# Performance work log

Hardware: AMD Instinct MI355X
Metric: run time of the kernel (lower is better)

The kernel has to match this reference:

```python
import jax, jax.numpy as jnp
import numpy as np

MARGIN = 1.0
EPS = 1e-12


def setup_inputs() -> dict:
    key = jax.random.key(0)
    k1, k2, k3 = jax.random.split(key, 3)
    inputs = jax.random.normal(k1, (8192, 128), dtype=jnp.float32)
    targets = jax.random.randint(k2, (8192,), 0, 64, dtype=jnp.int64)
    center = jax.random.normal(k3, (16, 128), dtype=jnp.float32)
    return {"inputs": inputs, "targets": targets, "center": center}


def reference(inputs, targets, center):
    n = inputs.shape[0]
    # pairwise Euclidean distances via ||a||^2 + ||b||^2 - 2 a.b  (matches addmm_ trick)
    sq = jnp.sum(inputs * inputs, axis=1)                      # [n]
    dist2 = sq[:, None] + sq[None, :] - 2.0 * (inputs @ inputs.T)
    dist = jnp.sqrt(jnp.clip(dist2, EPS))                      # [n, n]

    mask = targets[:, None] == targets[None, :]                # same-class mask [n, n]

    # batch-hard mining, fully vectorized (replaces per-row python loops)
    dist_ap = jnp.max(jnp.where(mask, dist, -jnp.inf), axis=1)  # hardest positive
    neg_min = jnp.min(jnp.where(mask, jnp.inf, dist), axis=1)   # hardest negative
    has_neg = jnp.any(~mask, axis=1)
    dist_an = jnp.where(has_neg, neg_min, dist_ap + MARGIN)

    # center augmentation: min over distances to L2-normalized prototypes
    cn = center / jnp.linalg.norm(center, axis=1, keepdims=True)       # [P, d]
    dc = jnp.sqrt(jnp.sum((inputs[:, None, :] - cn[None, :, :]) ** 2, axis=-1))  # [n, P]
    dc = jnp.clip(dc, EPS)
    dist_an = jnp.minimum(dist_an, jnp.min(dc, axis=1))

    # MarginRankingLoss with y=1: mean(relu(dist_ap - dist_an + margin))
    loss = jnp.mean(jnp.maximum(dist_ap - dist_an + MARGIN, 0.0))
    return loss
```

## Files before the change

### kernel.cpp

```cpp
#include <hip/hip_runtime.h>
#include <hip/hip_bf16.h>


#define N_ROWS 8192
#define DIM 128
#define NPROTO 16
#define MARGIN_F 1.0f
#define EPS_F 1e-12f

typedef __attribute__((ext_vector_type(8))) short short8;
typedef __attribute__((ext_vector_type(4))) float float4v;

static __device__ __forceinline__ unsigned f2bf(float f) {
  unsigned u = __float_as_uint(f);
  u += 0x7fffu + ((u >> 16) & 1u);
  return u >> 16;
}

__global__ void prep_centers_kernel(const float* __restrict__ center,
                                    float* __restrict__ cn,
                                    float* __restrict__ out0) {
  int tid = threadIdx.x;
  if (tid == 0) out0[0] = 0.0f;
  int row = tid >> 4;
  int l = tid & 15;
  float v[8];
  float ss = 0.f;
#pragma unroll
  for (int j = 0; j < 8; ++j) {
    v[j] = center[row * DIM + l * 8 + j];
    ss += v[j] * v[j];
  }
#pragma unroll
  for (int m = 1; m < 16; m <<= 1) ss += __shfl_xor(ss, m, 64);
  float inv = 1.0f / sqrtf(ss);
#pragma unroll
  for (int j = 0; j < 8; ++j) cn[row * DIM + l * 8 + j] = v[j] * inv;
}

__global__ void prep_rows_kernel(const float* __restrict__ x,
                                 const float* __restrict__ cn,
                                 uint4* __restrict__ xbf4,
                                 float* __restrict__ sq,
                                 float* __restrict__ mindc) {
  __shared__ float scn[NPROTO * DIM];
  int tid = threadIdx.x;
#pragma unroll
  for (int j = 0; j < 8; ++j) scn[j * 256 + tid] = cn[j * 256 + tid];
  __syncthreads();
  int rloc = tid >> 4, l = tid & 15;
  int row = blockIdx.x * 16 + rloc;
  float4 v0 = ((const float4*)x)[row * 32 + l * 2];
  float4 v1 = ((const float4*)x)[row * 32 + l * 2 + 1];
  float ss = v0.x * v0.x + v0.y * v0.y + v0.z * v0.z + v0.w * v0.w +
             v1.x * v1.x + v1.y * v1.y + v1.z * v1.z + v1.w * v1.w;
  float dots[NPROTO];
#pragma unroll
  for (int p = 0; p < NPROTO; ++p) {
    const float* c = &scn[p * DIM + l * 8];
    dots[p] = v0.x * c[0] + v0.y * c[1] + v0.z * c[2] + v0.w * c[3] +
              v1.x * c[4] + v1.y * c[5] + v1.z * c[6] + v1.w * c[7];
  }
#pragma unroll
  for (int m = 1; m < 16; m <<= 1) {
    ss += __shfl_xor(ss, m, 64);
#pragma unroll
    for (int p = 0; p < NPROTO; ++p) dots[p] += __shfl_xor(dots[p], m, 64);
  }
  uint4 pk;
  pk.x = f2bf(v0.x) | (f2bf(v0.y) << 16);
  pk.y = f2bf(v0.z) | (f2bf(v0.w) << 16);
  pk.z = f2bf(v1.x) | (f2bf(v1.y) << 16);
  pk.w = f2bf(v1.z) | (f2bf(v1.w) << 16);
  xbf4[row * 16 + l] = pk;
  if (l == 0) {
    float mind2 = INFINITY;
#pragma unroll
    for (int p = 0; p < NPROTO; ++p)
      mind2 = fminf(mind2, ss + 1.0f - 2.0f * dots[p]);
    sq[row] = ss;
    mindc[row] = fmaxf(sqrtf(fmaxf(mind2, 0.0f)), EPS_F);
  }
}

__global__ __launch_bounds__(256, 2) void
pairdist_kernel(const char* __restrict__ xbf, const float* __restrict__ sq,
                const int* __restrict__ tgt, float* __restrict__ pmax,
                float* __restrict__ pmin) {
  __shared__ float smax[4][64];
  __shared__ float smin[4][64];
  int bid = blockIdx.x;
  int rg = bid >> 3;
  int strip = bid & 7;
  int wave = threadIdx.x >> 6, lane = threadIdx.x & 63;
  int rowbase = rg * 64;
  int q = lane >> 4, l16 = lane & 15;
  int colbase = strip * 1024 + wave * 256;

  short8 a[4][4];
#pragma unroll
  for (int rt = 0; rt < 4; ++rt) {
    const char* ar = xbf + (size_t)(rowbase + rt * 16 + l16) * 256 + q * 16;
#pragma unroll
    for (int kc = 0; kc < 4; ++kc) a[rt][kc] = *(const short8*)(ar + kc * 64);
  }
  int4 trow[4];
#pragma unroll
  for (int rt = 0; rt < 4; ++rt)
    trow[rt] = ((const int4*)tgt)[(rowbase >> 2) + rt * 4 + q];

  float maxp[16], minn[16];
#pragma unroll
  for (int i = 0; i < 16; ++i) { maxp[i] = -INFINITY; minn[i] = INFINITY; }

  short8 bn[4];
  float sqn;
  int tcn;
  {
    const char* br = xbf + (size_t)(colbase + l16) * 256 + q * 16;
#pragma unroll
    for (int kc = 0; kc < 4; ++kc) bn[kc] = *(const short8*)(br + kc * 64);
    sqn = sq[colbase + l16];
    tcn = tgt[colbase + l16];
  }

#pragma unroll
  for (int t = 0; t < 16; ++t) {
    short8 bc[4];
#pragma unroll
    for (int kc = 0; kc < 4; ++kc) bc[kc] = bn[kc];
    float sqc = sqn;
    int tc = tcn;
    int cnext = colbase + ((t + 1) & 15) * 16;
    const char* br = xbf + (size_t)(cnext + l16) * 256 + q * 16;
#pragma unroll
    for (int kc = 0; kc < 4; ++kc) bn[kc] = *(const short8*)(br + kc * 64);
    sqn = sq[cnext + l16];
    tcn = tgt[cnext + l16];

    float4v acc[4];
#pragma unroll
    for (int rt = 0; rt < 4; ++rt) acc[rt] = (float4v){0.f, 0.f, 0.f, 0.f};
#pragma unroll
    for (int kc = 0; kc < 4; ++kc)
#pragma unroll
      for (int rt = 0; rt < 4; ++rt)
        acc[rt] = __builtin_amdgcn_mfma_f32_16x16x32_bf16(a[rt][kc], bc[kc],
                                                          acc[rt], 0, 0, 0);
#pragma unroll
    for (int rt = 0; rt < 4; ++rt) {
      int tr[4] = {trow[rt].x, trow[rt].y, trow[rt].z, trow[rt].w};
#pragma unroll
      for (int r = 0; r < 4; ++r) {
        float v = fmaf(-2.0f, acc[rt][r], sqc);
        bool s = (tc == tr[r]);
        int idx = rt * 4 + r;
        maxp[idx] = s ? fmaxf(maxp[idx], v) : maxp[idx];
        minn[idx] = s ? minn[idx] : fminf(minn[idx], v);
      }
    }
  }

#pragma unroll
  for (int m = 1; m < 16; m <<= 1) {
#pragma unroll
    for (int i = 0; i < 16; ++i) {
      maxp[i] = fmaxf(maxp[i], __shfl_xor(maxp[i], m, 64));
      minn[i] = fminf(minn[i], __shfl_xor(minn[i], m, 64));
    }
  }
  if (l16 == 0) {
#pragma unroll
    for (int rt = 0; rt < 4; ++rt)
#pragma unroll
      for (int r = 0; r < 4; ++r) {
        smax[wave][rt * 16 + q * 4 + r] = maxp[rt * 4 + r];
        smin[wave][rt * 16 + q * 4 + r] = minn[rt * 4 + r];
      }
  }
  __syncthreads();
  if (threadIdx.x < 64) {
    float M = fmaxf(fmaxf(smax[0][threadIdx.x], smax[1][threadIdx.x]),
                    fmaxf(smax[2][threadIdx.x], smax[3][threadIdx.x]));
    float m = fminf(fminf(smin[0][threadIdx.x], smin[1][threadIdx.x]),
                    fminf(smin[2][threadIdx.x], smin[3][threadIdx.x]));
    pmax[strip * N_ROWS + rowbase + threadIdx.x] = M;
    pmin[strip * N_ROWS + rowbase + threadIdx.x] = m;
  }
}

__global__ void finalize_kernel(const float* __restrict__ pmax,
                                const float* __restrict__ pmin,
                                const float* __restrict__ sq,
                                const float* __restrict__ mindc,
                                float* __restrict__ out) {
  __shared__ float wsum[4];
  int i = blockIdx.x * 256 + threadIdx.x;
  float maxv = -INFINITY, minv = INFINITY;
#pragma unroll
  for (int s = 0; s < 8; ++s) {
    maxv = fmaxf(maxv, pmax[s * N_ROWS + i]);
    minv = fminf(minv, pmin[s * N_ROWS + i]);
  }
  float si = sq[i];
  float dap = sqrtf(fmaxf(si + maxv, EPS_F));
  float dan = (minv > 1e37f) ? (dap + MARGIN_F) : sqrtf(fmaxf(si + minv, EPS_F));
  dan = fminf(dan, mindc[i]);
  float c = fmaxf(dap - dan + MARGIN_F, 0.0f) * (1.0f / (float)N_ROWS);
#pragma unroll
  for (int m = 1; m < 64; m <<= 1) c += __shfl_xor(c, m, 64);
  int lane = threadIdx.x & 63, wave = threadIdx.x >> 6;
  if (lane == 0) wsum[wave] = c;
  __syncthreads();
  if (threadIdx.x == 0) atomicAdd(out, wsum[0] + wsum[1] + wsum[2] + wsum[3]);
}

extern "C" void kernel_launch(void* const* d_in, const int* in_sizes, int n_in,
                              void* d_out, int out_size, void* d_ws, size_t ws_size,
                              hipStream_t stream) {
  const float* inputs = (const float*)d_in[0];
  const int* targets = (const int*)d_in[1];
  const float* center = (const float*)d_in[2];
  char* ws = (char*)d_ws;
  uint4* xbf4     = (uint4*)(ws + 0);
  float* sq       = (float*)(ws + 2097152);
  float* mindc    = (float*)(ws + 2129920);
  float* cn       = (float*)(ws + 2162688);
  float* pmax     = (float*)(ws + 2170880);
  float* pmin     = (float*)(ws + 2433024);
  float* out      = (float*)d_out;

  prep_centers_kernel<<<1, 256, 0, stream>>>(center, cn, out);
  prep_rows_kernel<<<512, 256, 0, stream>>>(inputs, cn, xbf4, sq, mindc);
  pairdist_kernel<<<1024, 256, 0, stream>>>((const char*)xbf4, sq, targets, pmax, pmin);
  finalize_kernel<<<32, 256, 0, stream>>>(pmax, pmin, sq, mindc, out);
}
```

Baseline: 111.4 us.

## Encode class mask into extra GEMM K-dims, stage column tiles via LDS

Each row gets 64 extra bf16 K-columns holding a one-hot class code scaled so that same-class pairs pick up a large bias in the dot product. A plain max and min over the biased distances then separates positives from negatives without per-element target compares, and finalize removes the bias. Column tiles are now loaded into swizzled, double-buffered LDS with global_load_lds and shared by four waves. The center prep kernel is merged into the row prep kernel. The cost is a K dimension of 192 instead of 128 (50% more MFMA work), per-tile block barriers, and a bias of 32768 that coarsens fp32 precision of the positive distances.

```diff
diff --git a/kernel.cpp b/kernel.cpp
--- a/kernel.cpp
+++ b/kernel.cpp
@@ -1,15 +1,18 @@
 #include <hip/hip_runtime.h>
-#include <hip/hip_bf16.h>
 
 
 #define N_ROWS 8192
 #define DIM 128
+#define KDIM 192
+#define ROWB 384
 #define NPROTO 16
 #define MARGIN_F 1.0f
 #define EPS_F 1e-12f
+#define BIAS_F 32768.0f
 
 typedef __attribute__((ext_vector_type(8))) short short8;
 typedef __attribute__((ext_vector_type(4))) float float4v;
+typedef __attribute__((ext_vector_type(4))) unsigned uint4v;
 
 static __device__ __forceinline__ unsigned f2bf(float f) {
   unsigned u = __float_as_uint(f);
@@ -17,38 +20,39 @@
   return u >> 16;
 }
 
-__global__ void prep_centers_kernel(const float* __restrict__ center,
-                                    float* __restrict__ cn,
-                                    float* __restrict__ out0) {
-  int tid = threadIdx.x;
-  if (tid == 0) out0[0] = 0.0f;
-  int row = tid >> 4;
-  int l = tid & 15;
-  float v[8];
-  float ss = 0.f;
-#pragma unroll
-  for (int j = 0; j < 8; ++j) {
-    v[j] = center[row * DIM + l * 8 + j];
-    ss += v[j] * v[j];
-  }
-#pragma unroll
-  for (int m = 1; m < 16; m <<= 1) ss += __shfl_xor(ss, m, 64);
-  float inv = 1.0f / sqrtf(ss);
-#pragma unroll
-  for (int j = 0; j < 8; ++j) cn[row * DIM + l * 8 + j] = v[j] * inv;
-}
-
-__global__ void prep_rows_kernel(const float* __restrict__ x,
-                                 const float* __restrict__ cn,
-                                 uint4* __restrict__ xbf4,
-                                 float* __restrict__ sq,
-                                 float* __restrict__ mindc) {
+static __device__ __forceinline__ void gload_lds16(const void* g, void* l) {
+  __builtin_amdgcn_global_load_lds(
+      (const __attribute__((address_space(1))) unsigned*)g,
+      (__attribute__((address_space(3))) unsigned*)l, 16, 0, 0);
+}
+
+__global__ void prep_kernel(const float* __restrict__ x,
+                            const float* __restrict__ center,
+                            const int* __restrict__ tgt,
+                            char* __restrict__ xbf,
+                            float* __restrict__ sq,
+                            float* __restrict__ mindc,
+                            float* __restrict__ out) {
   __shared__ float scn[NPROTO * DIM];
   int tid = threadIdx.x;
-#pragma unroll
-  for (int j = 0; j < 8; ++j) scn[j * 256 + tid] = cn[j * 256 + tid];
+  if (blockIdx.x == 0 && tid == 0) out[0] = 0.0f;
+  int rloc = tid >> 4, l = tid & 15;
+  {
+    float v[8];
+    float ss = 0.f;
+#pragma unroll
+    for (int j = 0; j < 8; ++j) {
+      v[j] = center[rloc * DIM + l * 8 + j];
+      ss += v[j] * v[j];
+    }
+#pragma unroll
+    for (int m = 1; m < 16; m <<= 1) ss += __shfl_xor(ss, m, 64);
+    float inv = 1.0f / sqrtf(ss);
+#pragma unroll
+    for (int j = 0; j < 8; ++j) scn[rloc * DIM + l * 8 + j] = v[j] * inv;
+  }
   __syncthreads();
-  int rloc = tid >> 4, l = tid & 15;
+
   int row = blockIdx.x * 16 + rloc;
   float4 v0 = ((const float4*)x)[row * 32 + l * 2];
   float4 v1 = ((const float4*)x)[row * 32 + l * 2 + 1];
@@ -72,7 +76,17 @@
   pk.y = f2bf(v0.z) | (f2bf(v0.w) << 16);
   pk.z = f2bf(v1.x) | (f2bf(v1.y) << 16);
   pk.w = f2bf(v1.z) | (f2bf(v1.w) << 16);
-  xbf4[row * 16 + l] = pk;
+  *(uint4*)(xbf + (size_t)row * ROWB + l * 16) = pk;
+  int cls = tgt[row];
+  if (l < 8) {
+    unsigned wv = (cls & 1) ? 0xC3000000u : 0x0000C300u;
+    uint4 oh;
+    oh.x = ((cls >> 1) == (l * 4 + 0)) ? wv : 0u;
+    oh.y = ((cls >> 1) == (l * 4 + 1)) ? wv : 0u;
+    oh.z = ((cls >> 1) == (l * 4 + 2)) ? wv : 0u;
+    oh.w = ((cls >> 1) == (l * 4 + 3)) ? wv : 0u;
+    *(uint4*)(xbf + (size_t)row * ROWB + 256 + l * 16) = oh;
+  }
   if (l == 0) {
     float mind2 = INFINITY;
 #pragma unroll
@@ -85,107 +99,109 @@
 
 __global__ __launch_bounds__(256, 2) void
 pairdist_kernel(const char* __restrict__ xbf, const float* __restrict__ sq,
-                const int* __restrict__ tgt, float* __restrict__ pmax,
-                float* __restrict__ pmin) {
-  __shared__ float smax[4][64];
-  __shared__ float smin[4][64];
-  int bid = blockIdx.x;
-  int rg = bid >> 3;
-  int strip = bid & 7;
-  int wave = threadIdx.x >> 6, lane = threadIdx.x & 63;
-  int rowbase = rg * 64;
-  int q = lane >> 4, l16 = lane & 15;
-  int colbase = strip * 1024 + wave * 256;
-
-  short8 a[4][4];
+                float* __restrict__ pmax, float* __restrict__ pmin) {
+  __shared__ __align__(16) char bl[2][6144];
+  const int bid = blockIdx.x;
+  const int rg = bid >> 4;
+  const int strip = bid & 15;
+  const int wave = threadIdx.x >> 6, lane = threadIdx.x & 63;
+  const int q = lane >> 4, l16 = lane & 15;
+  const int rowbase = rg * 256 + wave * 64;
+  const int stripbase = strip * 512;
+
+  const int slot = wave * 64 + lane;
+  const char* const srcstrip = xbf + (size_t)stripbase * ROWB;
+  int op0 = slot * 16;
+  int c0 = op0 / ROWB;
+  const int soff0 = c0 * ROWB + ((op0 - c0 * ROWB) ^ ((c0 & 7) << 4));
+  int op1 = 4096 + slot * 16;
+  int c1 = op1 / ROWB;
+  const int soff1 = c1 * ROWB + ((op1 - c1 * ROWB) ^ ((c1 & 7) << 4));
+
+  auto stage = [&](int t, char* buf) {
+    const char* s = srcstrip + (size_t)t * 6144;
+    gload_lds16(s + soff0, buf + wave * 1024);
+    if (wave < 2) gload_lds16(s + soff1, buf + 4096 + wave * 1024);
+  };
+
+  stage(0, bl[0]);
+
+  short8 a[4][6];
 #pragma unroll
   for (int rt = 0; rt < 4; ++rt) {
-    const char* ar = xbf + (size_t)(rowbase + rt * 16 + l16) * 256 + q * 16;
-#pragma unroll
-    for (int kc = 0; kc < 4; ++kc) a[rt][kc] = *(const short8*)(ar + kc * 64);
-  }
-  int4 trow[4];
-#pragma unroll
-  for (int rt = 0; rt < 4; ++rt)
-    trow[rt] = ((const int4*)tgt)[(rowbase >> 2) + rt * 4 + q];
+    const char* ar = xbf + (size_t)(rowbase + rt * 16 + l16) * ROWB + q * 16;
+#pragma unroll
+    for (int kc = 0; kc < 6; ++kc) a[rt][kc] = *(const short8*)(ar + kc * 64);
+#pragma unroll
+    for (int kc = 4; kc < 6; ++kc) {
+      uint4v u = __builtin_bit_cast(uint4v, a[rt][kc]);
+      u ^= 0x80008000u;
+      a[rt][kc] = __builtin_bit_cast(short8, u);
+    }
+  }
+
+  int roff[6];
+#pragma unroll
+  for (int kc = 0; kc < 6; ++kc)
+    roff[kc] = (l16 * ROWB + kc * 64 + q * 16) ^ ((l16 & 7) << 4);
 
   float maxp[16], minn[16];
 #pragma unroll
-  for (int i = 0; i < 16; ++i) { maxp[i] = -INFINITY; minn[i] = INFINITY; }
-
-  short8 bn[4];
-  float sqn;
-  int tcn;
-  {
-    const char* br = xbf + (size_t)(colbase + l16) * 256 + q * 16;
-#pragma unroll
-    for (int kc = 0; kc < 4; ++kc) bn[kc] = *(const short8*)(br + kc * 64);
-    sqn = sq[colbase + l16];
-    tcn = tgt[colbase + l16];
-  }
-
-#pragma unroll
-  for (int t = 0; t < 16; ++t) {
-    short8 bc[4];
-#pragma unroll
-    for (int kc = 0; kc < 4; ++kc) bc[kc] = bn[kc];
-    float sqc = sqn;
-    int tc = tcn;
-    int cnext = colbase + ((t + 1) & 15) * 16;
-    const char* br = xbf + (size_t)(cnext + l16) * 256 + q * 16;
-#pragma unroll
-    for (int kc = 0; kc < 4; ++kc) bn[kc] = *(const short8*)(br + kc * 64);
-    sqn = sq[cnext + l16];
-    tcn = tgt[cnext + l16];
-
+  for (int i = 0; i < 16; ++i) {
+    maxp[i] = -INFINITY;
+    minn[i] = INFINITY;
+  }
+
+  auto tile_step = [&](int t, const char* cur, char* nxt) {
+    __syncthreads();
+    if (t + 1 < 32) stage(t + 1, nxt);
+    float sqc = sq[stripbase + t * 16 + l16];
+    short8 b[6];
+#pragma unroll
+    for (int kc = 0; kc < 6; ++kc) b[kc] = *(const short8*)(cur + roff[kc]);
     float4v acc[4];
 #pragma unroll
     for (int rt = 0; rt < 4; ++rt) acc[rt] = (float4v){0.f, 0.f, 0.f, 0.f};
 #pragma unroll
-    for (int kc = 0; kc < 4; ++kc)
+    for (int kc = 0; kc < 6; ++kc)
 #pragma unroll
       for (int rt = 0; rt < 4; ++rt)
-        acc[rt] = __builtin_amdgcn_mfma_f32_16x16x32_bf16(a[rt][kc], bc[kc],
+        acc[rt] = __builtin_amdgcn_mfma_f32_16x16x32_bf16(a[rt][kc], b[kc],
                                                           acc[rt], 0, 0, 0);
 #pragma unroll
-    for (int rt = 0; rt < 4; ++rt) {
-      int tr[4] = {trow[rt].x, trow[rt].y, trow[rt].z, trow[rt].w};
+    for (int rt = 0; rt < 4; ++rt)
 #pragma unroll
       for (int r = 0; r < 4; ++r) {
         float v = fmaf(-2.0f, acc[rt][r], sqc);
-        bool s = (tc == tr[r]);
         int idx = rt * 4 + r;
-        maxp[idx] = s ? fmaxf(maxp[idx], v) : maxp[idx];
-        minn[idx] = s ? minn[idx] : fminf(minn[idx], v);
+        maxp[idx] = fmaxf(maxp[idx], v);
+        minn[idx] = fminf(minn[idx], v);
       }
-    }
-  }
-
-#pragma unroll
-  for (int m = 1; m < 16; m <<= 1) {
+  };
+
+#pragma unroll 1
+  for (int tp = 0; tp < 16; ++tp) {
+    tile_step(2 * tp, bl[0], bl[1]);
+    tile_step(2 * tp + 1, bl[1], bl[0]);
+  }
+
+#pragma unroll
+  for (int m = 1; m < 16; m <<= 1)
 #pragma unroll
     for (int i = 0; i < 16; ++i) {
       maxp[i] = fmaxf(maxp[i], __shfl_xor(maxp[i], m, 64));
       minn[i] = fminf(minn[i], __shfl_xor(minn[i], m, 64));
     }
-  }
   if (l16 == 0) {
+    float* pM = pmax + (size_t)strip * N_ROWS + rowbase + q * 4;
+    float* pm = pmin + (size_t)strip * N_ROWS + rowbase + q * 4;
 #pragma unroll
     for (int rt = 0; rt < 4; ++rt)
 #pragma unroll
       for (int r = 0; r < 4; ++r) {
-        smax[wave][rt * 16 + q * 4 + r] = maxp[rt * 4 + r];
-        smin[wave][rt * 16 + q * 4 + r] = minn[rt * 4 + r];
+        pM[rt * 16 + r] = maxp[rt * 4 + r];
+        pm[rt * 16 + r] = minn[rt * 4 + r];
       }
-  }
-  __syncthreads();
-  if (threadIdx.x < 64) {
-    float M = fmaxf(fmaxf(smax[0][threadIdx.x], smax[1][threadIdx.x]),
-                    fmaxf(smax[2][threadIdx.x], smax[3][threadIdx.x]));
-    float m = fminf(fminf(smin[0][threadIdx.x], smin[1][threadIdx.x]),
-                    fminf(smin[2][threadIdx.x], smin[3][threadIdx.x]));
-    pmax[strip * N_ROWS + rowbase + threadIdx.x] = M;
-    pmin[strip * N_ROWS + rowbase + threadIdx.x] = m;
   }
 }
 
@@ -198,19 +214,20 @@
   int i = blockIdx.x * 256 + threadIdx.x;
   float maxv = -INFINITY, minv = INFINITY;
 #pragma unroll
-  for (int s = 0; s < 8; ++s) {
+  for (int s = 0; s < 16; ++s) {
     maxv = fmaxf(maxv, pmax[s * N_ROWS + i]);
     minv = fminf(minv, pmin[s * N_ROWS + i]);
   }
   float si = sq[i];
-  float dap = sqrtf(fmaxf(si + maxv, EPS_F));
-  float dan = (minv > 1e37f) ? (dap + MARGIN_F) : sqrtf(fmaxf(si + minv, EPS_F));
+  float dap = sqrtf(fmaxf(si + (maxv - BIAS_F), EPS_F));
+  float dan = (minv > 16384.0f) ? (dap + MARGIN_F)
+                                : sqrtf(fmaxf(si + minv, EPS_F));
   dan = fminf(dan, mindc[i]);
   float c = fmaxf(dap - dan + MARGIN_F, 0.0f) * (1.0f / (float)N_ROWS);
 #pragma unroll
   for (int m = 1; m < 64; m <<= 1) c += __shfl_xor(c, m, 64);
-  int lane = threadIdx.x & 63, wave = threadIdx.x >> 6;
-  if (lane == 0) wsum[wave] = c;
+  int lane = threadIdx.x & 63, wv = threadIdx.x >> 6;
+  if (lane == 0) wsum[wv] = c;
   __syncthreads();
   if (threadIdx.x == 0) atomicAdd(out, wsum[0] + wsum[1] + wsum[2] + wsum[3]);
 }
@@ -222,16 +239,14 @@
   const int* targets = (const int*)d_in[1];
   const float* center = (const float*)d_in[2];
   char* ws = (char*)d_ws;
-  uint4* xbf4     = (uint4*)(ws + 0);
-  float* sq       = (float*)(ws + 2097152);
-  float* mindc    = (float*)(ws + 2129920);
-  float* cn       = (float*)(ws + 2162688);
-  float* pmax     = (float*)(ws + 2170880);
-  float* pmin     = (float*)(ws + 2433024);
-  float* out      = (float*)d_out;
-
-  prep_centers_kernel<<<1, 256, 0, stream>>>(center, cn, out);
-  prep_rows_kernel<<<512, 256, 0, stream>>>(inputs, cn, xbf4, sq, mindc);
-  pairdist_kernel<<<1024, 256, 0, stream>>>((const char*)xbf4, sq, targets, pmax, pmin);
+  char* xbf    = ws;
+  float* sq    = (float*)(ws + 3145728);
+  float* mindc = (float*)(ws + 3178496);
+  float* pmax  = (float*)(ws + 3211264);
+  float* pmin  = (float*)(ws + 3735552);
+  float* out   = (float*)d_out;
+
+  prep_kernel<<<512, 256, 0, stream>>>(inputs, center, targets, xbf, sq, mindc, out);
+  pairdist_kernel<<<512, 256, 0, stream>>>(xbf, sq, pmax, pmin);
   finalize_kernel<<<32, 256, 0, stream>>>(pmax, pmin, sq, mindc, out);
 }
```

Result: faster. 99.39 us (-10.8%).
